# Performance work log

Hardware: AMD Instinct MI355X
Metric: run time of the kernel (lower is better)

The kernel has to match this reference:

```python
import jax, jax.numpy as jnp
import numpy as np


def _dwconv(x, w, pad):
    # depthwise conv, NCHW, weight (C,1,kh,kw), feature_group_count=C
    return jax.lax.conv_general_dilated(
        x, w, window_strides=(1, 1), padding=pad,
        feature_group_count=x.shape[1],
        dimension_numbers=('NCHW', 'OIHW', 'NCHW'))


def _max_channel_relu(x):
    # assumed MaxChannelReLU: keep only the channel-max value at each (b,h,w)
    return x * (x == jnp.max(x, axis=1, keepdims=True))


def setup_inputs() -> dict:
    key = jax.random.key(0)
    ks = jax.random.split(key, 6)
    B, C, H, W = 16, 64, 128, 128
    x = jax.random.normal(ks[0], (B, C, H, W), dtype=jnp.float32)
    w_bbx = 0.1 * jax.random.normal(ks[1], (C, 1, 1, 1), dtype=jnp.float32)
    w_width = 0.1 * jax.random.normal(ks[2], (C, 1, 1, 11), dtype=jnp.float32)
    w_width_sh = 0.1 * jax.random.normal(ks[3], (C, 1, 1, 1), dtype=jnp.float32)
    w_height = 0.1 * jax.random.normal(ks[4], (C, 1, 11, 1), dtype=jnp.float32)
    w_height_sh = 0.1 * jax.random.normal(ks[5], (C, 1, 1, 1), dtype=jnp.float32)
    return {"x": x, "w_bbx": w_bbx, "w_width": w_width,
            "w_width_sh": w_width_sh, "w_height": w_height,
            "w_height_sh": w_height_sh}


def reference(x, w_bbx, w_width, w_width_sh, w_height, w_height_sh):
    B, C, H, W = x.shape
    # self.bbx: depthwise 1x1 conv == per-channel scale
    wh = x * w_bbx.reshape(1, C, 1, 1)
    # width branch: depthwise (1,11) conv pad 5, scaled by W, then shared 1x1
    w = _dwconv(wh, w_width, [(0, 0), (5, 5)]) * W
    w = w * w_width_sh.reshape(1, C, 1, 1)
    # height branch: depthwise (11,1) conv pad 5, scaled by H, then shared 1x1
    h = _dwconv(wh, w_height, [(5, 5), (0, 0)]) * H
    h = h * w_height_sh.reshape(1, C, 1, 1)
    sx = jax.nn.sigmoid(x)
    M = jnp.max(sx, axis=(-2, -1), keepdims=True) - 0.01
    score = x * (sx > M).astype(x.dtype)
    S = jnp.sum(score, axis=(-2, -1), keepdims=True)
    sn = score / S  # normalized weights, reused by all weighted reductions
    ws = jnp.sum(w * sn, axis=(-2, -1))
    hs = jnp.sum(h * sn, axis=(-2, -1))
    ps = jnp.max(sx, axis=(-2, -1))
    col = jnp.arange(W, dtype=x.dtype).reshape(1, 1, 1, W)
    row = jnp.arange(H, dtype=x.dtype).reshape(1, 1, H, 1)
    x1 = jnp.sum(col * sn, axis=(-2, -1)) - ws / 2
    y1 = jnp.sum(row * sn, axis=(-2, -1)) - hs / 2
    x2 = x1 + ws
    y2 = y1 + hs
    score_m = _max_channel_relu(score)
    w_m = _max_channel_relu(w)
    h_m = _max_channel_relu(h)
    i = jnp.broadcast_to(jnp.arange(B, dtype=x.dtype)[:, None], (B, C))
    bbox = jnp.stack([i, x1, y1, x2, y2, ps], axis=-1).reshape(-1, 6)
    return jnp.concatenate([score_m, w_m, h_m], axis=1), bbox
```

## Files before the change

### kernel.cpp

```cpp
#include <hip/hip_runtime.h>
#include <math.h>

#define BATCH 16
#define CH    64
#define HH    128
#define WW    128
#define PLANE (HH*WW)
#define OUT0  (BATCH*3*CH*PLANE)
#define SR4    36
#define TSROWS 18
#define T16R   26
#define PART_OFF 2048
#define MB_OFF   90112
#define MB_N     786432

typedef float f4v __attribute__((ext_vector_type(4)));


__device__ __forceinline__ unsigned enc32(float f) {
    unsigned u = __float_as_uint(f);
    return (u & 0x80000000u) ? ~u : (u | 0x80000000u);
}
__device__ __forceinline__ float dec32(unsigned k) {
    unsigned u = (k & 0x80000000u) ? (k ^ 0x80000000u) : ~k;
    return __uint_as_float(u);
}

__global__ __launch_bounds__(256) void k_max(const float* __restrict__ x,
                                             float* __restrict__ ws) {
    int bid = blockIdx.x;
    int tid = threadIdx.x;
    const float4* xp = (const float4*)(x + (size_t)bid * PLANE);
    float m = -INFINITY;
#pragma unroll
    for (int i = 0; i < 16; i++) {
        float4 v = xp[i * 256 + tid];
        m = fmaxf(m, fmaxf(fmaxf(v.x, v.y), fmaxf(v.z, v.w)));
    }
#pragma unroll
    for (int off = 32; off; off >>= 1) m = fmaxf(m, __shfl_xor(m, off, 64));
    __shared__ float sm[4];
    int wid = tid >> 6, lane = tid & 63;
    if (lane == 0) sm[wid] = m;
    __syncthreads();
    if (tid == 0) {
        float mm = fmaxf(fmaxf(sm[0], sm[1]), fmaxf(sm[2], sm[3]));
        float ps = 1.0f / (1.0f + expf(-mm));
        ws[bid] = ps - 0.01f;
        ws[1024 + bid] = ps;
    }
}

__global__ __launch_bounds__(256, 1) void k_conv16(
    const float* __restrict__ x,
    const float* __restrict__ w_bbx, const float* __restrict__ w_width,
    const float* __restrict__ w_width_sh, const float* __restrict__ w_height,
    const float* __restrict__ w_height_sh,
    const float* __restrict__ ws, float* __restrict__ wsums,
    unsigned long long* __restrict__ mb) {
    __shared__ float4 xs4[2][T16R * SR4];
    __shared__ float red[16 * 4 * 5];
    int bid = blockIdx.x;
    int xcd = bid & 7, kk = (bid >> 3) & 7, t = bid >> 6;
    int gb = xcd * 8 + kk;
    int g = gb & 3, b = gb >> 2;
    int tid = threadIdx.x;
    int r = tid >> 5, q = tid & 31;
    int wid = tid >> 6, lane = tid & 63;

    for (int j = tid; j < 2 * T16R * SR4; j += 256)
        ((float4*)xs4)[j] = make_float4(0.f, 0.f, 0.f, 0.f);
    __syncthreads();
    int cbase = g * 16;
    {
        const float* xp = x + (size_t)(b * 64 + cbase) * PLANE;
        for (int j = tid; j < T16R * 32; j += 256) {
            int i = j >> 5, c4 = j & 31;
            int gr = t * 16 - 5 + i;
            float4 v = make_float4(0.f, 0.f, 0.f, 0.f);
            if ((unsigned)gr < 128u) v = ((const float4*)xp)[gr * 32 + c4];
            xs4[0][i * SR4 + 2 + c4] = v;
        }
    }
    unsigned long long kS[2][4], kW[2][4], kH[2][4];
#pragma unroll
    for (int rr = 0; rr < 2; rr++)
#pragma unroll
        for (int j = 0; j < 4; j++) { kS[rr][j] = 0; kW[rr][j] = 0; kH[rr][j] = 0; }

    int cur = 0;
    for (int cc = 0; cc < 16; cc++) {
        __syncthreads();
        int c = cbase + cc;
        float4 p0 = make_float4(0,0,0,0), p1 = p0, p2 = p0, p3 = p0;
        bool have = (cc + 1 < 16);
        int i0 = tid >> 5, c4 = tid & 31;
        if (have) {
            const float* xp = x + (size_t)(b * 64 + c + 1) * PLANE;
            int gr0 = t * 16 - 5 + i0;
            if ((unsigned)gr0 < 128u) p0 = ((const float4*)xp)[gr0 * 32 + c4];
            int gr1 = gr0 + 8;
            if ((unsigned)gr1 < 128u) p1 = ((const float4*)xp)[gr1 * 32 + c4];
            int gr2 = gr0 + 16;
            if ((unsigned)gr2 < 128u) p2 = ((const float4*)xp)[gr2 * 32 + c4];
            if (tid < 64) {
                int gr3 = gr0 + 24;
                if ((unsigned)gr3 < 128u) p3 = ((const float4*)xp)[gr3 * 32 + c4];
            }
        }
        float wkc[11], hkc[11];
#pragma unroll
        for (int k = 0; k < 11; k++) {
            wkc[k] = w_width[c * 11 + k];
            hkc[k] = w_height[c * 11 + k];
        }
        float cb = w_bbx[c];
        float cw = 128.0f * w_width_sh[c] * cb;
        float chs = 128.0f * w_height_sh[c] * cb;
        float M = ws[b * 64 + c];

        float a0x=0,a0y=0,a0z=0,a0w=0, a1x=0,a1y=0,a1z=0,a1w=0;
        float4 vx0, vx1;
#pragma unroll
        for (int k = 0; k < 12; k++) {
            float4 v = xs4[cur][(2 * r + k) * SR4 + 2 + q];
            if (k == 5) vx0 = v;
            if (k == 6) vx1 = v;
            if (k < 11) {
                float h = hkc[k];
                a0x += v.x*h; a0y += v.y*h; a0z += v.z*h; a0w += v.w*h;
            }
            if (k >= 1) {
                float h = hkc[k-1];
                a1x += v.x*h; a1y += v.y*h; a1z += v.z*h; a1w += v.w*h;
            }
        }
        float ho[2][4] = {{a0x*chs, a0y*chs, a0z*chs, a0w*chs},
                          {a1x*chs, a1y*chs, a1z*chs, a1w*chs}};
        float S = 0.f, Sw = 0.f, Sh = 0.f, Scol = 0.f, Srow = 0.f;
#pragma unroll
        for (int rr = 0; rr < 2; rr++) {
            float4 vc = (rr == 0) ? vx0 : vx1;
            int srow = (2 * r + 5 + rr) * SR4 + q;
            float4 b0 = xs4[cur][srow + 0];
            float4 b1 = xs4[cur][srow + 1];
            float4 b3 = xs4[cur][srow + 3];
            float4 b4 = xs4[cur][srow + 4];
            float wbuf[20] = {b0.x,b0.y,b0.z,b0.w, b1.x,b1.y,b1.z,b1.w,
                              vc.x,vc.y,vc.z,vc.w, b3.x,b3.y,b3.z,b3.w,
                              b4.x,b4.y,b4.z,b4.w};
            float xv[4] = {vc.x, vc.y, vc.z, vc.w};
            float s4 = 0.f;
#pragma unroll
            for (int j = 0; j < 4; j++) {
                float acc = 0.f;
#pragma unroll
                for (int k = 0; k < 11; k++) acc += wbuf[j + 3 + k] * wkc[k];
                float wo = acc * cw;
                float sx = 1.0f / (1.0f + expf(-xv[j]));
                float sc = (sx > M) ? xv[j] : 0.0f;
                s4 += sc;
                Sw += wo * sc;
                Sh += ho[rr][j] * sc;
                Scol += (float)(4 * q + j) * sc;
                unsigned long long cand;
                cand = ((unsigned long long)enc32(sc) << 32) | (unsigned)c;
                if (cand > kS[rr][j]) kS[rr][j] = cand;
                cand = ((unsigned long long)enc32(wo) << 32) | (unsigned)c;
                if (cand > kW[rr][j]) kW[rr][j] = cand;
                cand = ((unsigned long long)enc32(ho[rr][j]) << 32) | (unsigned)c;
                if (cand > kH[rr][j]) kH[rr][j] = cand;
            }
            S += s4;
            Srow += (float)(t * 16 + 2 * r + rr) * s4;
        }
#pragma unroll
        for (int off = 32; off; off >>= 1) {
            S    += __shfl_xor(S, off, 64);
            Sw   += __shfl_xor(Sw, off, 64);
            Sh   += __shfl_xor(Sh, off, 64);
            Scol += __shfl_xor(Scol, off, 64);
            Srow += __shfl_xor(Srow, off, 64);
        }
        if (lane == 0) {
            float* rr2 = &red[(cc * 4 + wid) * 5];
            rr2[0] = S; rr2[1] = Sw; rr2[2] = Sh; rr2[3] = Scol; rr2[4] = Srow;
        }
        if (have) {
            xs4[cur ^ 1][i0 * SR4 + 2 + c4] = p0;
            xs4[cur ^ 1][(i0 + 8) * SR4 + 2 + c4] = p1;
            xs4[cur ^ 1][(i0 + 16) * SR4 + 2 + c4] = p2;
            if (tid < 64) xs4[cur ^ 1][(i0 + 24) * SR4 + 2 + c4] = p3;
        }
        cur ^= 1;
    }
    __syncthreads();
    if (tid < 80) {
        int cc = tid / 5, j = tid % 5;
        float s = red[(cc * 4 + 0) * 5 + j] + red[(cc * 4 + 1) * 5 + j]
                + red[(cc * 4 + 2) * 5 + j] + red[(cc * 4 + 3) * 5 + j];
        int c = cbase + cc;
        wsums[(((size_t)(b * 64 + c)) * 8 + t) * 5 + j] = s;
    }
    int y0 = t * 16 + 2 * r;
    size_t pix = (size_t)y0 * 128 + 4 * q;
    unsigned long long* o = mb + (size_t)g * MB_N;
    size_t i0s = (size_t)(b * 3 + 0) * 16384 + pix;
    size_t i1s = (size_t)(b * 3 + 1) * 16384 + pix;
    size_t i2s = (size_t)(b * 3 + 2) * 16384 + pix;
#pragma unroll
    for (int rr = 0; rr < 2; rr++)
#pragma unroll
        for (int j = 0; j < 4; j++) {
            o[i0s + rr * 128 + j] = kS[rr][j];
            o[i1s + rr * 128 + j] = kW[rr][j];
            o[i2s + rr * 128 + j] = kH[rr][j];
        }
}

template <int CPG>
__global__ __launch_bounds__(256) void k_conv(
    const float* __restrict__ x,
    const float* __restrict__ w_bbx, const float* __restrict__ w_width,
    const float* __restrict__ w_width_sh, const float* __restrict__ w_height,
    const float* __restrict__ w_height_sh,
    const float* __restrict__ ws, float* __restrict__ wsums,
    unsigned long long* __restrict__ mb) {
    __shared__ float4 xs4[2][TSROWS * SR4];
    __shared__ float red[CPG * 4 * 5];
    int t = blockIdx.x, g = blockIdx.y, b = blockIdx.z;
    int tid = threadIdx.x;
    int r = tid >> 5, q = tid & 31;
    int wid = tid >> 6, lane = tid & 63;
    for (int j = tid; j < 2 * TSROWS * SR4; j += 256)
        ((float4*)xs4)[j] = make_float4(0.f, 0.f, 0.f, 0.f);
    __syncthreads();
    int cbase = g * CPG;
    {
        const float* xp = x + (size_t)(b * 64 + cbase) * PLANE;
        for (int j = tid; j < TSROWS * 32; j += 256) {
            int i = j >> 5, c4 = j & 31;
            int gr = t * 8 - 5 + i;
            float4 v = make_float4(0.f, 0.f, 0.f, 0.f);
            if ((unsigned)gr < 128u) v = ((const float4*)xp)[gr * 32 + c4];
            xs4[0][i * SR4 + 2 + c4] = v;
        }
    }
    unsigned long long kW[4], kH[4], kS[4];
#pragma unroll
    for (int j = 0; j < 4; j++) { kW[j] = 0ull; kH[j] = 0ull; kS[j] = 0ull; }
    int cur = 0;
    for (int cc = 0; cc < CPG; cc++) {
        __syncthreads();
        int c = cbase + cc;
        float4 p0 = make_float4(0,0,0,0), p1 = p0, p2 = p0;
        bool have = (cc + 1 < CPG);
        if (have) {
            const float* xp = x + (size_t)(b * 64 + c + 1) * PLANE;
            int i0 = tid >> 5, c4 = tid & 31;
            int g0 = t * 8 - 5 + i0;
            if ((unsigned)g0 < 128u) p0 = ((const float4*)xp)[g0 * 32 + c4];
            int g1 = g0 + 8;
            if ((unsigned)g1 < 128u) p1 = ((const float4*)xp)[g1 * 32 + c4];
            if (tid < 64) {
                int g2 = g0 + 16;
                if ((unsigned)g2 < 128u) p2 = ((const float4*)xp)[g2 * 32 + c4];
            }
        }
        float wkc[11], hkc[11];
#pragma unroll
        for (int k = 0; k < 11; k++) {
            wkc[k] = w_width[c * 11 + k];
            hkc[k] = w_height[c * 11 + k];
        }
        float cb = w_bbx[c];
        float cw = 128.0f * w_width_sh[c] * cb;
        float chs = 128.0f * w_height_sh[c] * cb;
        float M = ws[b * 64 + c];
        float4 vx;
        float hx = 0.f, hy = 0.f, hz = 0.f, hw = 0.f;
#pragma unroll
        for (int k = 0; k < 11; k++) {
            float4 v = xs4[cur][(r + k) * SR4 + 2 + q];
            if (k == 5) vx = v;
            hx += v.x * hkc[k]; hy += v.y * hkc[k];
            hz += v.z * hkc[k]; hw += v.w * hkc[k];
        }
        float wbuf[20];
        {
            float4 a0 = xs4[cur][(r + 5) * SR4 + q + 0];
            float4 a1 = xs4[cur][(r + 5) * SR4 + q + 1];
            float4 a3 = xs4[cur][(r + 5) * SR4 + q + 3];
            float4 a4 = xs4[cur][(r + 5) * SR4 + q + 4];
            wbuf[0]=a0.x; wbuf[1]=a0.y; wbuf[2]=a0.z; wbuf[3]=a0.w;
            wbuf[4]=a1.x; wbuf[5]=a1.y; wbuf[6]=a1.z; wbuf[7]=a1.w;
            wbuf[8]=vx.x; wbuf[9]=vx.y; wbuf[10]=vx.z; wbuf[11]=vx.w;
            wbuf[12]=a3.x; wbuf[13]=a3.y; wbuf[14]=a3.z; wbuf[15]=a3.w;
            wbuf[16]=a4.x; wbuf[17]=a4.y; wbuf[18]=a4.z; wbuf[19]=a4.w;
        }
        float wo[4];
#pragma unroll
        for (int j = 0; j < 4; j++) {
            float acc = 0.f;
#pragma unroll
            for (int k = 0; k < 11; k++) acc += wbuf[j + 3 + k] * wkc[k];
            wo[j] = acc * cw;
        }
        float ho[4] = {hx * chs, hy * chs, hz * chs, hw * chs};
        float xv[4] = {vx.x, vx.y, vx.z, vx.w};
        float S = 0.f, Sw = 0.f, Sh = 0.f, Scol = 0.f, Srow = 0.f;
#pragma unroll
        for (int j = 0; j < 4; j++) {
            float sx = 1.0f / (1.0f + expf(-xv[j]));
            float sc = (sx > M) ? xv[j] : 0.0f;
            S += sc; Sw += wo[j] * sc; Sh += ho[j] * sc;
            Scol += (float)(4 * q + j) * sc;
            unsigned long long cand;
            cand = ((unsigned long long)enc32(sc) << 32) | (unsigned)c;
            if (cand > kS[j]) kS[j] = cand;
            cand = ((unsigned long long)enc32(wo[j]) << 32) | (unsigned)c;
            if (cand > kW[j]) kW[j] = cand;
            cand = ((unsigned long long)enc32(ho[j]) << 32) | (unsigned)c;
            if (cand > kH[j]) kH[j] = cand;
        }
        Srow = (float)(t * 8 + r) * S;
#pragma unroll
        for (int off = 32; off; off >>= 1) {
            S    += __shfl_xor(S, off, 64);
            Sw   += __shfl_xor(Sw, off, 64);
            Sh   += __shfl_xor(Sh, off, 64);
            Scol += __shfl_xor(Scol, off, 64);
            Srow += __shfl_xor(Srow, off, 64);
        }
        if (lane == 0) {
            float* rr = &red[(cc * 4 + wid) * 5];
            rr[0] = S; rr[1] = Sw; rr[2] = Sh; rr[3] = Scol; rr[4] = Srow;
        }
        if (have) {
            int i0 = tid >> 5, c4 = tid & 31;
            xs4[cur ^ 1][i0 * SR4 + 2 + c4] = p0;
            xs4[cur ^ 1][(i0 + 8) * SR4 + 2 + c4] = p1;
            if (tid < 64) xs4[cur ^ 1][(i0 + 16) * SR4 + 2 + c4] = p2;
        }
        cur ^= 1;
    }
    __syncthreads();
    if (tid < CPG * 5) {
        int cc = tid / 5, j = tid % 5;
        float s = red[(cc * 4 + 0) * 5 + j] + red[(cc * 4 + 1) * 5 + j]
                + red[(cc * 4 + 2) * 5 + j] + red[(cc * 4 + 3) * 5 + j];
        int c = cbase + cc;
        wsums[(((size_t)(b * 64 + c)) * 16 + t) * 5 + j] = s;
    }
    int gr = t * 8 + r;
    size_t pix = (size_t)gr * 128 + 4 * q;
    unsigned long long* o = mb + (size_t)g * MB_N;
    size_t i0 = (size_t)(b * 3 + 0) * 16384 + pix;
    size_t i1 = (size_t)(b * 3 + 1) * 16384 + pix;
    size_t i2 = (size_t)(b * 3 + 2) * 16384 + pix;
#pragma unroll
    for (int j = 0; j < 4; j++) {
        o[i0 + j] = kS[j];
        o[i1 + j] = kW[j];
        o[i2 + j] = kH[j];
    }
}

template <int NG>
__global__ __launch_bounds__(256) void k_scatter(
    const unsigned long long* __restrict__ mb, float* __restrict__ out) {
    int chunk = blockIdx.x;
    int f = blockIdx.y;
    int b = blockIdx.z;
    int tid = threadIdx.x;
    size_t pix = (size_t)chunk * 1024 + tid * 4;
    size_t ki = (size_t)(b * 3 + f) * 16384 + pix;
    float val[4];
    int win[4];
#pragma unroll
    for (int j = 0; j < 4; j++) {
        unsigned long long k = 0ull;
#pragma unroll
        for (int g2 = 0; g2 < NG; g2++) {
            unsigned long long kg = mb[(size_t)g2 * MB_N + ki + j];
            if (kg > k) k = kg;
        }
        val[j] = dec32((unsigned)(k >> 32));
        win[j] = (int)(k & 63u);
    }
    float* ob = out + (size_t)(b * 192 + f * 64) * PLANE + pix;
#pragma unroll
    for (int c = 0; c < 64; c++) {
        f4v o;
        o.x = (win[0] == c) ? val[0] : 0.f;
        o.y = (win[1] == c) ? val[1] : 0.f;
        o.z = (win[2] == c) ? val[2] : 0.f;
        o.w = (win[3] == c) ? val[3] : 0.f;
        __builtin_nontemporal_store(o, (f4v*)&ob[(size_t)c * PLANE]);
    }
}

template <int NT>
__global__ __launch_bounds__(256) void k_bbox(const float* __restrict__ ws,
                                              float* __restrict__ out) {
    int idx = blockIdx.x * 256 + threadIdx.x;
    if (idx >= 1024) return;
    int b = idx >> 6;
    const float* p = ws + PART_OFF + (size_t)idx * (NT * 5);
    float S = 0.f, Sw = 0.f, Sh = 0.f, Scol = 0.f, Srow = 0.f;
#pragma unroll
    for (int t = 0; t < NT; t++) {
        S    += p[t * 5 + 0];
        Sw   += p[t * 5 + 1];
        Sh   += p[t * 5 + 2];
        Scol += p[t * 5 + 3];
        Srow += p[t * 5 + 4];
    }
    float ps = ws[1024 + idx];
    float inv = 1.0f / S;
    float wsv = Sw * inv, hsv = Sh * inv;
    float x1 = Scol * inv - 0.5f * wsv;
    float y1 = Srow * inv - 0.5f * hsv;
    float* o = out + OUT0 + (size_t)idx * 6;
    o[0] = (float)b;
    o[1] = x1;
    o[2] = y1;
    o[3] = x1 + wsv;
    o[4] = y1 + hsv;
    o[5] = ps;
}

extern "C" void kernel_launch(void* const* d_in, const int* in_sizes, int n_in,
                              void* d_out, int out_size, void* d_ws, size_t ws_size,
                              hipStream_t stream) {
    const float* x          = (const float*)d_in[0];
    const float* w_bbx      = (const float*)d_in[1];
    const float* w_width    = (const float*)d_in[2];
    const float* w_width_sh = (const float*)d_in[3];
    const float* w_height   = (const float*)d_in[4];
    const float* w_height_sh= (const float*)d_in[5];
    float* out = (float*)d_out;
    float* ws  = (float*)d_ws;
    unsigned long long* mb = (unsigned long long*)(ws + MB_OFF);

    size_t need4 = (size_t)MB_OFF * 4 + 4ull * MB_N * 8ull;

    k_max<<<dim3(1024), dim3(256), 0, stream>>>(x, ws);
    if (ws_size >= need4) {
        k_conv16<<<dim3(512), dim3(256), 0, stream>>>(
            x, w_bbx, w_width, w_width_sh, w_height, w_height_sh,
            ws, ws + PART_OFF, mb);
        k_scatter<4><<<dim3(16, 3, 16), dim3(256), 0, stream>>>(mb, out);
        k_bbox<8><<<dim3(4), dim3(256), 0, stream>>>(ws, out);
    } else {
        k_conv<32><<<dim3(16, 2, 16), dim3(256), 0, stream>>>(
            x, w_bbx, w_width, w_width_sh, w_height, w_height_sh,
            ws, ws + PART_OFF, mb);
        k_scatter<2><<<dim3(16, 3, 16), dim3(256), 0, stream>>>(mb, out);
        k_bbox<16><<<dim3(4), dim3(256), 0, stream>>>(ws, out);
    }
}
```

Measured before the change: 338.0 us.

## Fuse max, conv, scatter and bbox into one cooperative kernel with grid syncs

Replaces the four-kernel pipeline (plane max, conv/argmax, scatter, bbox) with a single cooperative kernel of 512 blocks that separates the phases with grid.sync(). The goal is to remove kernel launch gaps and tail effects between stages. In exchange the grid is capped at co-resident occupancy, so the scatter phase loops over 768 virtual blocks on 512 real ones. Grid-wide barriers add their own cost. If the cooperative launch fails, the code falls back to the old multi-kernel path.

```diff
diff --git a/kernel.cpp b/kernel.cpp
--- a/kernel.cpp
+++ b/kernel.cpp
@@ -1,5 +1,8 @@
 #include <hip/hip_runtime.h>
+#include <hip/hip_cooperative_groups.h>
 #include <math.h>
+
+namespace cg = cooperative_groups;
 
 #define BATCH 16
 #define CH    64
@@ -24,6 +27,259 @@
 __device__ __forceinline__ float dec32(unsigned k) {
     unsigned u = (k & 0x80000000u) ? (k ^ 0x80000000u) : ~k;
     return __uint_as_float(u);
+}
+
+__global__ __launch_bounds__(256, 2) void k_fused(
+    const float* __restrict__ x,
+    const float* __restrict__ w_bbx, const float* __restrict__ w_width,
+    const float* __restrict__ w_width_sh, const float* __restrict__ w_height,
+    const float* __restrict__ w_height_sh,
+    float* __restrict__ ws, unsigned long long* __restrict__ mb,
+    float* __restrict__ out) {
+    __shared__ float4 xs4[2][T16R * SR4];
+    __shared__ float red[16 * 4 * 5];
+    cg::grid_group grid = cg::this_grid();
+    int bid = blockIdx.x;
+    int tid = threadIdx.x;
+    int wid = tid >> 6, lane = tid & 63;
+
+    for (int i2 = 0; i2 < 2; i2++) {
+        int p = bid * 2 + i2;
+        const float4* xp = (const float4*)(x + (size_t)p * PLANE);
+        float m = -INFINITY;
+#pragma unroll
+        for (int i = 0; i < 16; i++) {
+            float4 v = xp[i * 256 + tid];
+            m = fmaxf(m, fmaxf(fmaxf(v.x, v.y), fmaxf(v.z, v.w)));
+        }
+#pragma unroll
+        for (int off = 32; off; off >>= 1) m = fmaxf(m, __shfl_xor(m, off, 64));
+        if (lane == 0) red[wid] = m;
+        __syncthreads();
+        if (tid == 0) {
+            float mm = fmaxf(fmaxf(red[0], red[1]), fmaxf(red[2], red[3]));
+            float ps = 1.0f / (1.0f + expf(-mm));
+            ws[p] = ps - 0.01f;
+            ws[1024 + p] = ps;
+        }
+        __syncthreads();
+    }
+    grid.sync();
+
+    {
+        float* wsums = ws + PART_OFF;
+        int xcd = bid & 7, kk = (bid >> 3) & 7, t = bid >> 6;
+        int gb = xcd * 8 + kk;
+        int g = gb & 3, b = gb >> 2;
+        int r = tid >> 5, q = tid & 31;
+
+        for (int j = tid; j < 2 * T16R * SR4; j += 256)
+            ((float4*)xs4)[j] = make_float4(0.f, 0.f, 0.f, 0.f);
+        __syncthreads();
+        int cbase = g * 16;
+        {
+            const float* xp = x + (size_t)(b * 64 + cbase) * PLANE;
+            for (int j = tid; j < T16R * 32; j += 256) {
+                int i = j >> 5, c4 = j & 31;
+                int gr = t * 16 - 5 + i;
+                float4 v = make_float4(0.f, 0.f, 0.f, 0.f);
+                if ((unsigned)gr < 128u) v = ((const float4*)xp)[gr * 32 + c4];
+                xs4[0][i * SR4 + 2 + c4] = v;
+            }
+        }
+        unsigned long long kS[2][4], kW[2][4], kH[2][4];
+#pragma unroll
+        for (int rr = 0; rr < 2; rr++)
+#pragma unroll
+            for (int j = 0; j < 4; j++) { kS[rr][j] = 0; kW[rr][j] = 0; kH[rr][j] = 0; }
+
+        int cur = 0;
+        for (int cc = 0; cc < 16; cc++) {
+            __syncthreads();
+            int c = cbase + cc;
+            float4 p0 = make_float4(0,0,0,0), p1 = p0, p2 = p0, p3 = p0;
+            bool have = (cc + 1 < 16);
+            int i0 = tid >> 5, c4 = tid & 31;
+            if (have) {
+                const float* xp = x + (size_t)(b * 64 + c + 1) * PLANE;
+                int gr0 = t * 16 - 5 + i0;
+                if ((unsigned)gr0 < 128u) p0 = ((const float4*)xp)[gr0 * 32 + c4];
+                int gr1 = gr0 + 8;
+                if ((unsigned)gr1 < 128u) p1 = ((const float4*)xp)[gr1 * 32 + c4];
+                int gr2 = gr0 + 16;
+                if ((unsigned)gr2 < 128u) p2 = ((const float4*)xp)[gr2 * 32 + c4];
+                if (tid < 64) {
+                    int gr3 = gr0 + 24;
+                    if ((unsigned)gr3 < 128u) p3 = ((const float4*)xp)[gr3 * 32 + c4];
+                }
+            }
+            float wkc[11], hkc[11];
+#pragma unroll
+            for (int k = 0; k < 11; k++) {
+                wkc[k] = w_width[c * 11 + k];
+                hkc[k] = w_height[c * 11 + k];
+            }
+            float cb = w_bbx[c];
+            float cw = 128.0f * w_width_sh[c] * cb;
+            float chs = 128.0f * w_height_sh[c] * cb;
+            float M = ws[b * 64 + c];
+
+            float a0x=0,a0y=0,a0z=0,a0w=0, a1x=0,a1y=0,a1z=0,a1w=0;
+            float4 vx0, vx1;
+#pragma unroll
+            for (int k = 0; k < 12; k++) {
+                float4 v = xs4[cur][(2 * r + k) * SR4 + 2 + q];
+                if (k == 5) vx0 = v;
+                if (k == 6) vx1 = v;
+                if (k < 11) {
+                    float h = hkc[k];
+                    a0x += v.x*h; a0y += v.y*h; a0z += v.z*h; a0w += v.w*h;
+                }
+                if (k >= 1) {
+                    float h = hkc[k-1];
+                    a1x += v.x*h; a1y += v.y*h; a1z += v.z*h; a1w += v.w*h;
+                }
+            }
+            float ho[2][4] = {{a0x*chs, a0y*chs, a0z*chs, a0w*chs},
+                              {a1x*chs, a1y*chs, a1z*chs, a1w*chs}};
+            float S = 0.f, Sw = 0.f, Sh = 0.f, Scol = 0.f, Srow = 0.f;
+#pragma unroll
+            for (int rr = 0; rr < 2; rr++) {
+                float4 vc = (rr == 0) ? vx0 : vx1;
+                int srow = (2 * r + 5 + rr) * SR4 + q;
+                float4 b0 = xs4[cur][srow + 0];
+                float4 b1 = xs4[cur][srow + 1];
+                float4 b3 = xs4[cur][srow + 3];
+                float4 b4 = xs4[cur][srow + 4];
+                float wbuf[20] = {b0.x,b0.y,b0.z,b0.w, b1.x,b1.y,b1.z,b1.w,
+                                  vc.x,vc.y,vc.z,vc.w, b3.x,b3.y,b3.z,b3.w,
+                                  b4.x,b4.y,b4.z,b4.w};
+                float xv[4] = {vc.x, vc.y, vc.z, vc.w};
+                float s4 = 0.f;
+#pragma unroll
+                for (int j = 0; j < 4; j++) {
+                    float acc = 0.f;
+#pragma unroll
+                    for (int k = 0; k < 11; k++) acc += wbuf[j + 3 + k] * wkc[k];
+                    float wo = acc * cw;
+                    float sx = 1.0f / (1.0f + expf(-xv[j]));
+                    float sc = (sx > M) ? xv[j] : 0.0f;
+                    s4 += sc;
+                    Sw += wo * sc;
+                    Sh += ho[rr][j] * sc;
+                    Scol += (float)(4 * q + j) * sc;
+                    unsigned long long cand;
+                    cand = ((unsigned long long)enc32(sc) << 32) | (unsigned)c;
+                    if (cand > kS[rr][j]) kS[rr][j] = cand;
+                    cand = ((unsigned long long)enc32(wo) << 32) | (unsigned)c;
+                    if (cand > kW[rr][j]) kW[rr][j] = cand;
+                    cand = ((unsigned long long)enc32(ho[rr][j]) << 32) | (unsigned)c;
+                    if (cand > kH[rr][j]) kH[rr][j] = cand;
+                }
+                S += s4;
+                Srow += (float)(t * 16 + 2 * r + rr) * s4;
+            }
+#pragma unroll
+            for (int off = 32; off; off >>= 1) {
+                S    += __shfl_xor(S, off, 64);
+                Sw   += __shfl_xor(Sw, off, 64);
+                Sh   += __shfl_xor(Sh, off, 64);
+                Scol += __shfl_xor(Scol, off, 64);
+                Srow += __shfl_xor(Srow, off, 64);
+            }
+            if (lane == 0) {
+                float* rr2 = &red[(cc * 4 + wid) * 5];
+                rr2[0] = S; rr2[1] = Sw; rr2[2] = Sh; rr2[3] = Scol; rr2[4] = Srow;
+            }
+            if (have) {
+                xs4[cur ^ 1][i0 * SR4 + 2 + c4] = p0;
+                xs4[cur ^ 1][(i0 + 8) * SR4 + 2 + c4] = p1;
+                xs4[cur ^ 1][(i0 + 16) * SR4 + 2 + c4] = p2;
+                if (tid < 64) xs4[cur ^ 1][(i0 + 24) * SR4 + 2 + c4] = p3;
+            }
+            cur ^= 1;
+        }
+        __syncthreads();
+        if (tid < 80) {
+            int cc = tid / 5, j = tid % 5;
+            float s = red[(cc * 4 + 0) * 5 + j] + red[(cc * 4 + 1) * 5 + j]
+                    + red[(cc * 4 + 2) * 5 + j] + red[(cc * 4 + 3) * 5 + j];
+            int c = cbase + cc;
+            wsums[(((size_t)(b * 64 + c)) * 8 + t) * 5 + j] = s;
+        }
+        int y0 = t * 16 + 2 * r;
+        size_t pix = (size_t)y0 * 128 + 4 * q;
+        unsigned long long* o = mb + (size_t)g * MB_N;
+        size_t i0s = (size_t)(b * 3 + 0) * 16384 + pix;
+        size_t i1s = (size_t)(b * 3 + 1) * 16384 + pix;
+        size_t i2s = (size_t)(b * 3 + 2) * 16384 + pix;
+#pragma unroll
+        for (int rr = 0; rr < 2; rr++)
+#pragma unroll
+            for (int j = 0; j < 4; j++) {
+                o[i0s + rr * 128 + j] = kS[rr][j];
+                o[i1s + rr * 128 + j] = kW[rr][j];
+                o[i2s + rr * 128 + j] = kH[rr][j];
+            }
+    }
+    grid.sync();
+
+    for (int vb = bid; vb < 768; vb += 512) {
+        int chunk = vb & 15;
+        int f = (vb >> 4) % 3;
+        int b = vb / 48;
+        size_t pix = (size_t)chunk * 1024 + tid * 4;
+        size_t ki = (size_t)(b * 3 + f) * 16384 + pix;
+        float val[4];
+        int win[4];
+#pragma unroll
+        for (int j = 0; j < 4; j++) {
+            unsigned long long k = 0ull;
+#pragma unroll
+            for (int g2 = 0; g2 < 4; g2++) {
+                unsigned long long kg = mb[(size_t)g2 * MB_N + ki + j];
+                if (kg > k) k = kg;
+            }
+            val[j] = dec32((unsigned)(k >> 32));
+            win[j] = (int)(k & 63u);
+        }
+        float* ob = out + (size_t)(b * 192 + f * 64) * PLANE + pix;
+#pragma unroll
+        for (int c = 0; c < 64; c++) {
+            f4v o;
+            o.x = (win[0] == c) ? val[0] : 0.f;
+            o.y = (win[1] == c) ? val[1] : 0.f;
+            o.z = (win[2] == c) ? val[2] : 0.f;
+            o.w = (win[3] == c) ? val[3] : 0.f;
+            __builtin_nontemporal_store(o, (f4v*)&ob[(size_t)c * PLANE]);
+        }
+    }
+    if (bid < 4) {
+        int idx = bid * 256 + tid;
+        int b = idx >> 6;
+        const float* p = ws + PART_OFF + (size_t)idx * 40;
+        float S = 0.f, Sw = 0.f, Sh = 0.f, Scol = 0.f, Srow = 0.f;
+#pragma unroll
+        for (int t = 0; t < 8; t++) {
+            S    += p[t * 5 + 0];
+            Sw   += p[t * 5 + 1];
+            Sh   += p[t * 5 + 2];
+            Scol += p[t * 5 + 3];
+            Srow += p[t * 5 + 4];
+        }
+        float ps = ws[1024 + idx];
+        float inv = 1.0f / S;
+        float wsv = Sw * inv, hsv = Sh * inv;
+        float x1 = Scol * inv - 0.5f * wsv;
+        float y1 = Srow * inv - 0.5f * hsv;
+        float* o = out + OUT0 + (size_t)idx * 6;
+        o[0] = (float)b;
+        o[1] = x1;
+        o[2] = y1;
+        o[3] = x1 + wsv;
+        o[4] = y1 + hsv;
+        o[5] = ps;
+    }
 }
 
 __global__ __launch_bounds__(256) void k_max(const float* __restrict__ x,
@@ -118,7 +374,6 @@
         float cw = 128.0f * w_width_sh[c] * cb;
         float chs = 128.0f * w_height_sh[c] * cb;
         float M = ws[b * 64 + c];
-
         float a0x=0,a0y=0,a0z=0,a0w=0, a1x=0,a1y=0,a1z=0,a1w=0;
         float4 vx0, vx1;
 #pragma unroll
@@ -445,14 +700,22 @@
 
     size_t need4 = (size_t)MB_OFF * 4 + 4ull * MB_N * 8ull;
 
-    k_max<<<dim3(1024), dim3(256), 0, stream>>>(x, ws);
     if (ws_size >= need4) {
+        void* kargs[] = {(void*)&x, (void*)&w_bbx, (void*)&w_width,
+                         (void*)&w_width_sh, (void*)&w_height,
+                         (void*)&w_height_sh, (void*)&ws, (void*)&mb,
+                         (void*)&out};
+        hipError_t e = hipLaunchCooperativeKernel(
+            (void*)k_fused, dim3(512), dim3(256), kargs, 0, stream);
+        if (e == hipSuccess) return;
+        k_max<<<dim3(1024), dim3(256), 0, stream>>>(x, ws);
         k_conv16<<<dim3(512), dim3(256), 0, stream>>>(
             x, w_bbx, w_width, w_width_sh, w_height, w_height_sh,
             ws, ws + PART_OFF, mb);
         k_scatter<4><<<dim3(16, 3, 16), dim3(256), 0, stream>>>(mb, out);
         k_bbox<8><<<dim3(4), dim3(256), 0, stream>>>(ws, out);
     } else {
+        k_max<<<dim3(1024), dim3(256), 0, stream>>>(x, ws);
         k_conv<32><<<dim3(16, 2, 16), dim3(256), 0, stream>>>(
             x, w_bbx, w_width, w_width_sh, w_height, w_height_sh,
             ws, ws + PART_OFF, mb);
```

New measurement: 464.9 us. +37.5%, slower.

## Zero output via memset and scatter only channel-max winners; fuse bbox into scatter

Applied to the files above, without the earlier changes.

The output planes are now cleared with hipMemsetAsync, and the scatter kernel writes one value per pixel per branch, at the winning channel, instead of 64 nontemporal vector stores of mostly zeros. The separate bbox kernel is folded into the first four blocks of the scatter kernel, which removes one launch. The memset still writes the full 200MB output, so total traffic stays about the same. The winner stores are scattered scalar writes rather than coalesced vector stores.

```diff
diff --git a/kernel.cpp b/kernel.cpp
--- a/kernel.cpp
+++ b/kernel.cpp
@@ -118,7 +118,6 @@
         float cw = 128.0f * w_width_sh[c] * cb;
         float chs = 128.0f * w_height_sh[c] * cb;
         float M = ws[b * 64 + c];
-
         float a0x=0,a0y=0,a0z=0,a0w=0, a1x=0,a1y=0,a1z=0,a1w=0;
         float4 vx0, vx1;
 #pragma unroll
@@ -366,17 +365,18 @@
     }
 }
 
-template <int NG>
-__global__ __launch_bounds__(256) void k_scatter(
-    const unsigned long long* __restrict__ mb, float* __restrict__ out) {
-    int chunk = blockIdx.x;
-    int f = blockIdx.y;
-    int b = blockIdx.z;
+template <int NG, int NT>
+__global__ __launch_bounds__(256) void k_sparse(
+    const unsigned long long* __restrict__ mb, const float* __restrict__ ws,
+    float* __restrict__ out) {
+    int vb = blockIdx.x;
+    int chunk = vb & 15;
+    int f = (vb >> 4) % 3;
+    int b = vb / 48;
     int tid = threadIdx.x;
     size_t pix = (size_t)chunk * 1024 + tid * 4;
     size_t ki = (size_t)(b * 3 + f) * 16384 + pix;
-    float val[4];
-    int win[4];
+    float* ob = out + (size_t)(b * 192 + f * 64) * PLANE + pix;
 #pragma unroll
     for (int j = 0; j < 4; j++) {
         unsigned long long k = 0ull;
@@ -385,49 +385,36 @@
             unsigned long long kg = mb[(size_t)g2 * MB_N + ki + j];
             if (kg > k) k = kg;
         }
-        val[j] = dec32((unsigned)(k >> 32));
-        win[j] = (int)(k & 63u);
-    }
-    float* ob = out + (size_t)(b * 192 + f * 64) * PLANE + pix;
-#pragma unroll
-    for (int c = 0; c < 64; c++) {
-        f4v o;
-        o.x = (win[0] == c) ? val[0] : 0.f;
-        o.y = (win[1] == c) ? val[1] : 0.f;
-        o.z = (win[2] == c) ? val[2] : 0.f;
-        o.w = (win[3] == c) ? val[3] : 0.f;
-        __builtin_nontemporal_store(o, (f4v*)&ob[(size_t)c * PLANE]);
-    }
-}
-
-template <int NT>
-__global__ __launch_bounds__(256) void k_bbox(const float* __restrict__ ws,
-                                              float* __restrict__ out) {
-    int idx = blockIdx.x * 256 + threadIdx.x;
-    if (idx >= 1024) return;
-    int b = idx >> 6;
-    const float* p = ws + PART_OFF + (size_t)idx * (NT * 5);
-    float S = 0.f, Sw = 0.f, Sh = 0.f, Scol = 0.f, Srow = 0.f;
-#pragma unroll
-    for (int t = 0; t < NT; t++) {
-        S    += p[t * 5 + 0];
-        Sw   += p[t * 5 + 1];
-        Sh   += p[t * 5 + 2];
-        Scol += p[t * 5 + 3];
-        Srow += p[t * 5 + 4];
-    }
-    float ps = ws[1024 + idx];
-    float inv = 1.0f / S;
-    float wsv = Sw * inv, hsv = Sh * inv;
-    float x1 = Scol * inv - 0.5f * wsv;
-    float y1 = Srow * inv - 0.5f * hsv;
-    float* o = out + OUT0 + (size_t)idx * 6;
-    o[0] = (float)b;
-    o[1] = x1;
-    o[2] = y1;
-    o[3] = x1 + wsv;
-    o[4] = y1 + hsv;
-    o[5] = ps;
+        float val = dec32((unsigned)(k >> 32));
+        int win = (int)(k & 63u);
+        ob[(size_t)win * PLANE + j] = val;
+    }
+    if (vb < 4) {
+        int idx = vb * 256 + tid;
+        int bb = idx >> 6;
+        const float* p = ws + PART_OFF + (size_t)idx * (NT * 5);
+        float S = 0.f, Sw = 0.f, Sh = 0.f, Scol = 0.f, Srow = 0.f;
+#pragma unroll
+        for (int t = 0; t < NT; t++) {
+            S    += p[t * 5 + 0];
+            Sw   += p[t * 5 + 1];
+            Sh   += p[t * 5 + 2];
+            Scol += p[t * 5 + 3];
+            Srow += p[t * 5 + 4];
+        }
+        float ps = ws[1024 + idx];
+        float inv = 1.0f / S;
+        float wsv = Sw * inv, hsv = Sh * inv;
+        float x1 = Scol * inv - 0.5f * wsv;
+        float y1 = Srow * inv - 0.5f * hsv;
+        float* o = out + OUT0 + (size_t)idx * 6;
+        o[0] = (float)bb;
+        o[1] = x1;
+        o[2] = y1;
+        o[3] = x1 + wsv;
+        o[4] = y1 + hsv;
+        o[5] = ps;
+    }
 }
 
 extern "C" void kernel_launch(void* const* d_in, const int* in_sizes, int n_in,
@@ -445,18 +432,17 @@
 
     size_t need4 = (size_t)MB_OFF * 4 + 4ull * MB_N * 8ull;
 
+    hipMemsetAsync(out, 0, (size_t)OUT0 * sizeof(float), stream);
     k_max<<<dim3(1024), dim3(256), 0, stream>>>(x, ws);
     if (ws_size >= need4) {
         k_conv16<<<dim3(512), dim3(256), 0, stream>>>(
             x, w_bbx, w_width, w_width_sh, w_height, w_height_sh,
             ws, ws + PART_OFF, mb);
-        k_scatter<4><<<dim3(16, 3, 16), dim3(256), 0, stream>>>(mb, out);
-        k_bbox<8><<<dim3(4), dim3(256), 0, stream>>>(ws, out);
+        k_sparse<4, 8><<<dim3(768), dim3(256), 0, stream>>>(mb, ws, out);
     } else {
         k_conv<32><<<dim3(16, 2, 16), dim3(256), 0, stream>>>(
             x, w_bbx, w_width, w_width_sh, w_height, w_height_sh,
             ws, ws + PART_OFF, mb);
-        k_scatter<2><<<dim3(16, 3, 16), dim3(256), 0, stream>>>(mb, out);
-        k_bbox<16><<<dim3(4), dim3(256), 0, stream>>>(ws, out);
-    }
-}
+        k_sparse<2, 16><<<dim3(768), dim3(256), 0, stream>>>(mb, ws, out);
+    }
+}
```

After: 343.7 us. No clear change (+1.7%).
